# Optimization experiments

Measured on AMD Instinct MI355X. Metric: run time of the kernel, lower is better.

## Reference

```python
import jax, jax.numpy as jnp
import numpy as np

B, S, E, Q = 4, 4096, 1024, 8  # batch, seq, embed_dim, n_qubits


def setup_inputs() -> dict:
    key = jax.random.key(0)
    k1, k2, k3 = jax.random.split(key, 3)
    x = jax.random.normal(k1, (B, S, E), dtype=jnp.float32)
    W_enc = jax.random.normal(k2, (Q, E), dtype=jnp.float32) * (1.0 / np.sqrt(E))
    W_dec = jax.random.normal(k3, (E, Q), dtype=jnp.float32) * (1.0 / np.sqrt(Q))
    return {"x": x, "W_enc": W_enc, "W_dec": W_dec}


def reference(x, W_enc, W_dec):
    # encode tokens to rotation angles: [B,S,Q]
    angles = jnp.einsum('bse,qe->bsq', x, W_enc)
    c = jnp.cos(angles)
    # Analytic state-vector result of the circuit:
    #   RX(theta_i) on |0> then CNOT chain + ring closure, measure <Z_i>.
    # Heisenberg picture gives:
    #   <Z_0> = prod_{j=1..Q-1} cos(theta_j)
    #   <Z_i> = prod_{j=0..i}   cos(theta_j)   (i >= 1)
    p = jnp.cumprod(c, axis=-1)                      # prefix products
    q0 = jnp.prod(c[..., 1:], axis=-1, keepdims=True)
    q = jnp.concatenate([q0, p[..., 1:]], axis=-1)   # [B,S,Q] expvals
    # decode back to embed_dim and add residual
    return jnp.einsum('bsq,eq->bse', q, W_dec) + x
```

## Files before the change

kernel.cpp:

```cpp
#include <hip/hip_runtime.h>
#include <hip/hip_bf16.h>


typedef float v2f __attribute__((ext_vector_type(2)));
typedef float v4f __attribute__((ext_vector_type(4)));
typedef short bf16x8 __attribute__((ext_vector_type(8)));

#define EDIM 1024
#define QDIM 8
#define NTOK 16384
#define BLOCK 256
#define TOKPB 64
#define GRID (NTOK / TOKPB)
#define NKK (EDIM / 32)

__device__ __forceinline__ short f2bf(float f) {
    __hip_bfloat16 h = __float2bfloat16(f);
    return *reinterpret_cast<short*>(&h);
}

template<int K>
__device__ __forceinline__ float scan_mul_step(float p, int laneq) {
    int m = __builtin_amdgcn_update_dpp(0, __float_as_int(p), 0x110 | K, 0xF, 0xF, true);
    float tmul = (laneq >= K) ? __int_as_float(m) : 1.0f;
    return p * tmul;
}

__global__ __launch_bounds__(BLOCK)
void qattn_kernel(const float* __restrict__ x,
                  const float* __restrict__ W_enc,
                  const float* __restrict__ W_dec,
                  float* __restrict__ out)
{
    __shared__ short Blds[NKK * 64 * 8];
    __shared__ float qv_s[TOKPB][QDIM];

    const int t    = threadIdx.x;
    const int lane = t & 63;
    const int wave = t >> 6;
    const int tok0 = blockIdx.x * TOKPB;

#pragma unroll
    for (int s8 = 0; s8 < 8; ++s8) {
        const int s  = t * 8 + s8;
        const int kk = s >> 6;
        const int l  = s & 63;
        const int q  = l & 15;
        const int kg = l >> 4;
        bf16x8 bv;
        if (q < QDIM) {
            const float* wp = W_enc + q * EDIM + kk * 32 + kg * 8;
            v4f w0 = *(const v4f*)wp;
            v4f w1 = *(const v4f*)(wp + 4);
            bv[0] = f2bf(w0.x); bv[1] = f2bf(w0.y);
            bv[2] = f2bf(w0.z); bv[3] = f2bf(w0.w);
            bv[4] = f2bf(w1.x); bv[5] = f2bf(w1.y);
            bv[6] = f2bf(w1.z); bv[7] = f2bf(w1.w);
        } else {
            bv = (bf16x8){0, 0, 0, 0, 0, 0, 0, 0};
        }
        *(bf16x8*)&Blds[s * 8] = bv;
    }
    __syncthreads();

    const int wtok0 = tok0 + wave * 16;
    const int arow  = lane & 15;
    const int kg    = lane >> 4;

    v4f acc = (v4f){0.f, 0.f, 0.f, 0.f};
    const float* abase = x + (size_t)(wtok0 + arow) * EDIM + kg * 8;
#pragma unroll 8
    for (int kk = 0; kk < NKK; ++kk) {
        const float* ap = abase + kk * 32;
        v4f a0 = *(const v4f*)ap;
        v4f a1 = *(const v4f*)(ap + 4);
        bf16x8 av;
        av[0] = f2bf(a0.x); av[1] = f2bf(a0.y);
        av[2] = f2bf(a0.z); av[3] = f2bf(a0.w);
        av[4] = f2bf(a1.x); av[5] = f2bf(a1.y);
        av[6] = f2bf(a1.z); av[7] = f2bf(a1.w);
        bf16x8 bv = *(const bf16x8*)&Blds[(kk * 64 + lane) * 8];
        acc = __builtin_amdgcn_mfma_f32_16x16x32_bf16(av, bv, acc, 0, 0, 0);
    }

    const int q = lane & 15;
#pragma unroll
    for (int r = 0; r < 4; ++r) {
        const int ltok = wave * 16 + kg * 4 + r;
        float c = __cosf(acc[r]);

        float p = c;
        p = scan_mul_step<1>(p, q);
        p = scan_mul_step<2>(p, q);
        p = scan_mul_step<4>(p, q);

        float b = (q == 0) ? 1.0f : c;
        b = scan_mul_step<1>(b, q);
        b = scan_mul_step<2>(b, q);
        b = scan_mul_step<4>(b, q);

        if (q >= 1 && q < QDIM) qv_s[ltok][q] = p;
        if (q == 7)             qv_s[ltok][0] = b;
    }
    __syncthreads();

    const int e0 = t * 4;
    v4f wdlo[4], wdhi[4];
#pragma unroll
    for (int j = 0; j < 4; ++j) {
        wdlo[j] = *(const v4f*)(W_dec + (e0 + j) * QDIM);
        wdhi[j] = *(const v4f*)(W_dec + (e0 + j) * QDIM + 4);
    }

#pragma unroll 4
    for (int i = 0; i < TOKPB; ++i) {
        v4f qlo = *(const v4f*)&qv_s[i][0];
        v4f qhi = *(const v4f*)&qv_s[i][4];
        v4f xv  = *(const v4f*)(x + (size_t)(tok0 + i) * EDIM + e0);
        float od[4];
#pragma unroll
        for (int j = 0; j < 4; ++j) {
            v2f a = __builtin_elementwise_fma(
                        (v2f){qlo.x, qlo.y}, (v2f){wdlo[j].x, wdlo[j].y},
                        (v2f){xv[j], 0.f});
            a = __builtin_elementwise_fma((v2f){qlo.z, qlo.w},
                                          (v2f){wdlo[j].z, wdlo[j].w}, a);
            a = __builtin_elementwise_fma((v2f){qhi.x, qhi.y},
                                          (v2f){wdhi[j].x, wdhi[j].y}, a);
            a = __builtin_elementwise_fma((v2f){qhi.z, qhi.w},
                                          (v2f){wdhi[j].z, wdhi[j].w}, a);
            od[j] = a.x + a.y;
        }
        v4f o = (v4f){od[0], od[1], od[2], od[3]};
        __builtin_nontemporal_store(o, (v4f*)(out + (size_t)(tok0 + i) * EDIM + e0));
    }
}

extern "C" void kernel_launch(void* const* d_in, const int* in_sizes, int n_in,
                              void* d_out, int out_size, void* d_ws, size_t ws_size,
                              hipStream_t stream) {
    const float* x     = (const float*)d_in[0];
    const float* W_enc = (const float*)d_in[1];
    const float* W_dec = (const float*)d_in[2];
    float* out         = (float*)d_out;
    (void)d_ws; (void)ws_size;

    hipLaunchKernelGGL(qattn_kernel, dim3(GRID), dim3(BLOCK), 0, stream,
                       x, W_enc, W_dec, out);
}
```

Measured before the change: 35.99 us.

## Use MFMA for decode projection with per-wave tokens and drop block barrier

Replaces the scalar FMA decode stage with a bf16 16x16x32 MFMA per 16-column slice. Each wave now decodes only its own 16 tokens, using W_dec pre-converted to bf16 in LDS and padded with zeros to fill K=32, which removes the second block-wide barrier. Also adds an occupancy hint of two blocks per SM. The cost is scalar, strided per-element loads and stores of x/out (4 rows per lane at stride EDIM) instead of coalesced 16-byte vectors, and a loss of precision from bf16 rounding of q and W_dec.

Result: slower. 37.71 us (+4.8%).

```diff
diff --git a/kernel.cpp b/kernel.cpp
--- a/kernel.cpp
+++ b/kernel.cpp
@@ -13,6 +13,7 @@
 #define TOKPB 64
 #define GRID (NTOK / TOKPB)
 #define NKK (EDIM / 32)
+#define NET (EDIM / 16)
 
 __device__ __forceinline__ short f2bf(float f) {
     __hip_bfloat16 h = __float2bfloat16(f);
@@ -26,14 +27,16 @@
     return p * tmul;
 }
 
-__global__ __launch_bounds__(BLOCK)
+__global__ __launch_bounds__(BLOCK, 2)
 void qattn_kernel(const float* __restrict__ x,
                   const float* __restrict__ W_enc,
                   const float* __restrict__ W_dec,
                   float* __restrict__ out)
 {
-    __shared__ short Blds[NKK * 64 * 8];
-    __shared__ float qv_s[TOKPB][QDIM];
+    __shared__ short Benc[NKK * 64 * 8];
+    __shared__ short Bdec[EDIM * QDIM];
+    __shared__ short Bzero[8];
+    __shared__ float qv_w[4][16][QDIM];
 
     const int t    = threadIdx.x;
     const int lane = t & 63;
@@ -47,7 +50,7 @@
         const int l  = s & 63;
         const int q  = l & 15;
         const int kg = l >> 4;
-        bf16x8 bv;
+        bf16x8 bv = (bf16x8){0, 0, 0, 0, 0, 0, 0, 0};
         if (q < QDIM) {
             const float* wp = W_enc + q * EDIM + kk * 32 + kg * 8;
             v4f w0 = *(const v4f*)wp;
@@ -56,11 +59,22 @@
             bv[2] = f2bf(w0.z); bv[3] = f2bf(w0.w);
             bv[4] = f2bf(w1.x); bv[5] = f2bf(w1.y);
             bv[6] = f2bf(w1.z); bv[7] = f2bf(w1.w);
-        } else {
-            bv = (bf16x8){0, 0, 0, 0, 0, 0, 0, 0};
         }
-        *(bf16x8*)&Blds[s * 8] = bv;
+        *(bf16x8*)&Benc[s * 8] = bv;
     }
+#pragma unroll
+    for (int j = 0; j < 4; ++j) {
+        const int e = t * 4 + j;
+        v4f a = *(const v4f*)(W_dec + e * QDIM);
+        v4f b = *(const v4f*)(W_dec + e * QDIM + 4);
+        bf16x8 bv;
+        bv[0] = f2bf(a.x); bv[1] = f2bf(a.y);
+        bv[2] = f2bf(a.z); bv[3] = f2bf(a.w);
+        bv[4] = f2bf(b.x); bv[5] = f2bf(b.y);
+        bv[6] = f2bf(b.z); bv[7] = f2bf(b.w);
+        *(bf16x8*)&Bdec[e * 8] = bv;
+    }
+    if (t == 0) *(bf16x8*)&Bzero[0] = (bf16x8){0, 0, 0, 0, 0, 0, 0, 0};
     __syncthreads();
 
     const int wtok0 = tok0 + wave * 16;
@@ -79,14 +93,14 @@
         av[2] = f2bf(a0.z); av[3] = f2bf(a0.w);
         av[4] = f2bf(a1.x); av[5] = f2bf(a1.y);
         av[6] = f2bf(a1.z); av[7] = f2bf(a1.w);
-        bf16x8 bv = *(const bf16x8*)&Blds[(kk * 64 + lane) * 8];
+        bf16x8 bv = *(const bf16x8*)&Benc[(kk * 64 + lane) * 8];
         acc = __builtin_amdgcn_mfma_f32_16x16x32_bf16(av, bv, acc, 0, 0, 0);
     }
 
     const int q = lane & 15;
 #pragma unroll
     for (int r = 0; r < 4; ++r) {
-        const int ltok = wave * 16 + kg * 4 + r;
+        const int row = kg * 4 + r;
         float c = __cosf(acc[r]);
 
         float p = c;
@@ -99,40 +113,38 @@
         b = scan_mul_step<2>(b, q);
         b = scan_mul_step<4>(b, q);
 
-        if (q >= 1 && q < QDIM) qv_s[ltok][q] = p;
-        if (q == 7)             qv_s[ltok][0] = b;
-    }
-    __syncthreads();
-
-    const int e0 = t * 4;
-    v4f wdlo[4], wdhi[4];
-#pragma unroll
-    for (int j = 0; j < 4; ++j) {
-        wdlo[j] = *(const v4f*)(W_dec + (e0 + j) * QDIM);
-        wdhi[j] = *(const v4f*)(W_dec + (e0 + j) * QDIM + 4);
+        if (q >= 1 && q < QDIM) qv_w[wave][row][q] = p;
+        if (q == 7)             qv_w[wave][row][0] = b;
     }
 
-#pragma unroll 4
-    for (int i = 0; i < TOKPB; ++i) {
-        v4f qlo = *(const v4f*)&qv_s[i][0];
-        v4f qhi = *(const v4f*)&qv_s[i][4];
-        v4f xv  = *(const v4f*)(x + (size_t)(tok0 + i) * EDIM + e0);
-        float od[4];
-#pragma unroll
-        for (int j = 0; j < 4; ++j) {
-            v2f a = __builtin_elementwise_fma(
-                        (v2f){qlo.x, qlo.y}, (v2f){wdlo[j].x, wdlo[j].y},
-                        (v2f){xv[j], 0.f});
-            a = __builtin_elementwise_fma((v2f){qlo.z, qlo.w},
-                                          (v2f){wdlo[j].z, wdlo[j].w}, a);
-            a = __builtin_elementwise_fma((v2f){qhi.x, qhi.y},
-                                          (v2f){wdhi[j].x, wdhi[j].y}, a);
-            a = __builtin_elementwise_fma((v2f){qhi.z, qhi.w},
-                                          (v2f){wdhi[j].z, wdhi[j].w}, a);
-            od[j] = a.x + a.y;
-        }
-        v4f o = (v4f){od[0], od[1], od[2], od[3]};
-        __builtin_nontemporal_store(o, (v4f*)(out + (size_t)(tok0 + i) * EDIM + e0));
+    bf16x8 aq = (bf16x8){0, 0, 0, 0, 0, 0, 0, 0};
+    if (kg == 0) {
+        v4f lo = *(const v4f*)&qv_w[wave][arow][0];
+        v4f hi = *(const v4f*)&qv_w[wave][arow][4];
+        aq[0] = f2bf(lo.x); aq[1] = f2bf(lo.y);
+        aq[2] = f2bf(lo.z); aq[3] = f2bf(lo.w);
+        aq[4] = f2bf(hi.x); aq[5] = f2bf(hi.y);
+        aq[6] = f2bf(hi.z); aq[7] = f2bf(hi.w);
+    }
+
+    const size_t rbase = (size_t)(wtok0 + kg * 4) * EDIM;
+#pragma unroll 8
+    for (int j = 0; j < NET; ++j) {
+        const int e = j * 16 + arow;
+        bf16x8 bq = (kg == 0) ? *(const bf16x8*)&Bdec[e * 8]
+                              : *(const bf16x8*)&Bzero[0];
+        const float* xc = x + rbase + e;
+        v4f cf;
+        cf[0] = xc[0];
+        cf[1] = xc[EDIM];
+        cf[2] = xc[2 * EDIM];
+        cf[3] = xc[3 * EDIM];
+        v4f d = __builtin_amdgcn_mfma_f32_16x16x32_bf16(aq, bq, cf, 0, 0, 0);
+        float* oc = out + rbase + e;
+        oc[0]        = d[0];
+        oc[EDIM]     = d[1];
+        oc[2 * EDIM] = d[2];
+        oc[3 * EDIM] = d[3];
     }
 }
 
```

## Shrink blocks to 8 tokens and split K across waves with LDS reduction

Applied to the files above, without the earlier changes.

Each block now handles 8 tokens instead of 64. The four waves split the 1024-long reduction into quarters, and their partial MFMA results are combined through shared memory. W_enc is read straight from global memory instead of being staged in LDS, and W_dec loads are hoisted to the start. The goal is many more blocks for better latency hiding and less per-block setup. The cost is that half the MFMA lanes sit idle (only 8 of 16 rows are valid), plus extra barriers and a small cross-wave reduction.

After: 37.98 us. 1.06x slower.

```diff
diff --git a/kernel.cpp b/kernel.cpp
--- a/kernel.cpp
+++ b/kernel.cpp
@@ -10,9 +10,8 @@
 #define QDIM 8
 #define NTOK 16384
 #define BLOCK 256
-#define TOKPB 64
-#define GRID (NTOK / TOKPB)
-#define NKK (EDIM / 32)
+#define T 8
+#define GRID (NTOK / T)
 
 __device__ __forceinline__ short f2bf(float f) {
     __hip_bfloat16 h = __float2bfloat16(f);
@@ -26,68 +25,76 @@
     return p * tmul;
 }
 
-__global__ __launch_bounds__(BLOCK)
+__global__ __launch_bounds__(BLOCK, 2)
 void qattn_kernel(const float* __restrict__ x,
                   const float* __restrict__ W_enc,
                   const float* __restrict__ W_dec,
                   float* __restrict__ out)
 {
-    __shared__ short Blds[NKK * 64 * 8];
-    __shared__ float qv_s[TOKPB][QDIM];
+    __shared__ float red2[T][16][4];
+    __shared__ float qv_s[T][QDIM];
 
     const int t    = threadIdx.x;
     const int lane = t & 63;
     const int wave = t >> 6;
-    const int tok0 = blockIdx.x * TOKPB;
+    const int e0   = t * 4;
+    const int tok0 = blockIdx.x * T;
+
+    v4f wdlo[4], wdhi[4];
+#pragma unroll
+    for (int j = 0; j < 4; ++j) {
+        wdlo[j] = *(const v4f*)(W_dec + (e0 + j) * QDIM);
+        wdhi[j] = *(const v4f*)(W_dec + (e0 + j) * QDIM + 4);
+    }
+
+    const int r16  = lane & 15;
+    const int kg   = lane >> 4;
+    const bool ok  = (r16 < T);
+    const int koff = wave * 256 + kg * 8;
+
+    v4f acc = (v4f){0.f, 0.f, 0.f, 0.f};
+    const float* abase = x + (size_t)(tok0 + r16) * EDIM + koff;
+    const float* bbase = W_enc + (size_t)r16 * EDIM + koff;
 
 #pragma unroll
-    for (int s8 = 0; s8 < 8; ++s8) {
-        const int s  = t * 8 + s8;
-        const int kk = s >> 6;
-        const int l  = s & 63;
-        const int q  = l & 15;
-        const int kg = l >> 4;
-        bf16x8 bv;
-        if (q < QDIM) {
-            const float* wp = W_enc + q * EDIM + kk * 32 + kg * 8;
-            v4f w0 = *(const v4f*)wp;
-            v4f w1 = *(const v4f*)(wp + 4);
-            bv[0] = f2bf(w0.x); bv[1] = f2bf(w0.y);
-            bv[2] = f2bf(w0.z); bv[3] = f2bf(w0.w);
-            bv[4] = f2bf(w1.x); bv[5] = f2bf(w1.y);
-            bv[6] = f2bf(w1.z); bv[7] = f2bf(w1.w);
-        } else {
-            bv = (bf16x8){0, 0, 0, 0, 0, 0, 0, 0};
+    for (int kk = 0; kk < 8; ++kk) {
+        bf16x8 av = (bf16x8){0, 0, 0, 0, 0, 0, 0, 0};
+        bf16x8 bv = (bf16x8){0, 0, 0, 0, 0, 0, 0, 0};
+        if (ok) {
+            v4f a0 = *(const v4f*)(abase + kk * 32);
+            v4f a1 = *(const v4f*)(abase + kk * 32 + 4);
+            v4f b0 = *(const v4f*)(bbase + kk * 32);
+            v4f b1 = *(const v4f*)(bbase + kk * 32 + 4);
+            av[0] = f2bf(a0.x); av[1] = f2bf(a0.y);
+            av[2] = f2bf(a0.z); av[3] = f2bf(a0.w);
+            av[4] = f2bf(a1.x); av[5] = f2bf(a1.y);
+            av[6] = f2bf(a1.z); av[7] = f2bf(a1.w);
+            bv[0] = f2bf(b0.x); bv[1] = f2bf(b0.y);
+            bv[2] = f2bf(b0.z); bv[3] = f2bf(b0.w);
+            bv[4] = f2bf(b1.x); bv[5] = f2bf(b1.y);
+            bv[6] = f2bf(b1.z); bv[7] = f2bf(b1.w);
         }
-        *(bf16x8*)&Blds[s * 8] = bv;
-    }
-    __syncthreads();
-
-    const int wtok0 = tok0 + wave * 16;
-    const int arow  = lane & 15;
-    const int kg    = lane >> 4;
-
-    v4f acc = (v4f){0.f, 0.f, 0.f, 0.f};
-    const float* abase = x + (size_t)(wtok0 + arow) * EDIM + kg * 8;
-#pragma unroll 8
-    for (int kk = 0; kk < NKK; ++kk) {
-        const float* ap = abase + kk * 32;
-        v4f a0 = *(const v4f*)ap;
-        v4f a1 = *(const v4f*)(ap + 4);
-        bf16x8 av;
-        av[0] = f2bf(a0.x); av[1] = f2bf(a0.y);
-        av[2] = f2bf(a0.z); av[3] = f2bf(a0.w);
-        av[4] = f2bf(a1.x); av[5] = f2bf(a1.y);
-        av[6] = f2bf(a1.z); av[7] = f2bf(a1.w);
-        bf16x8 bv = *(const bf16x8*)&Blds[(kk * 64 + lane) * 8];
         acc = __builtin_amdgcn_mfma_f32_16x16x32_bf16(av, bv, acc, 0, 0, 0);
     }
 
-    const int q = lane & 15;
+    if (lane < 32) {
 #pragma unroll
-    for (int r = 0; r < 4; ++r) {
-        const int ltok = wave * 16 + kg * 4 + r;
-        float c = __cosf(acc[r]);
+        for (int r = 0; r < 4; ++r) {
+            const int row = kg * 4 + r;
+            red2[row][r16][wave] = acc[r];
+        }
+    }
+
+    asm volatile("s_waitcnt lgkmcnt(0)" ::: "memory");
+    __builtin_amdgcn_s_barrier();
+    __builtin_amdgcn_sched_barrier(0);
+
+    if (wave == 0) {
+        const int tk = lane >> 3;
+        const int q  = lane & 7;
+        v4f w4 = *(const v4f*)&red2[tk][q][0];
+        float s = (w4.x + w4.y) + (w4.z + w4.w);
+        float c = __cosf(s);
 
         float p = c;
         p = scan_mul_step<1>(p, q);
@@ -99,21 +106,16 @@
         b = scan_mul_step<2>(b, q);
         b = scan_mul_step<4>(b, q);
 
-        if (q >= 1 && q < QDIM) qv_s[ltok][q] = p;
-        if (q == 7)             qv_s[ltok][0] = b;
-    }
-    __syncthreads();
-
-    const int e0 = t * 4;
-    v4f wdlo[4], wdhi[4];
-#pragma unroll
-    for (int j = 0; j < 4; ++j) {
-        wdlo[j] = *(const v4f*)(W_dec + (e0 + j) * QDIM);
-        wdhi[j] = *(const v4f*)(W_dec + (e0 + j) * QDIM + 4);
+        if (q > 0)  qv_s[tk][q] = p;
+        if (q == 7) qv_s[tk][0] = b;
     }
 
-#pragma unroll 4
-    for (int i = 0; i < TOKPB; ++i) {
+    asm volatile("s_waitcnt lgkmcnt(0)" ::: "memory");
+    __builtin_amdgcn_s_barrier();
+    __builtin_amdgcn_sched_barrier(0);
+
+#pragma unroll
+    for (int i = 0; i < T; ++i) {
         v4f qlo = *(const v4f*)&qv_s[i][0];
         v4f qhi = *(const v4f*)&qv_s[i][4];
         v4f xv  = *(const v4f*)(x + (size_t)(tok0 + i) * EDIM + e0);
```
